# Kernel tuning notes

Measured on AMD Instinct MI355X. Metric: run time of the kernel, lower is better.

Reference implementation:

```python
import jax, jax.numpy as jnp
import numpy as np

NLAYERS, NHEAD, ATTN_LEN, DMODEL, DHID, NTOKEN = 9, 2, 5, 128, 512, 2
HD = DMODEL // NHEAD
B, T, F = 4, 4096, 128
INV_SQRT_HD = 1.0 / float(np.sqrt(HD))


def setup_inputs() -> dict:
    key = jax.random.key(0)
    ks = iter(jax.random.split(key, 64))
    def w(shape, s=0.02):
        return jax.random.normal(next(ks), shape, jnp.float32) * s
    return dict(
        x=jax.random.normal(next(ks), (B, T, F), jnp.float32),
        conv1_w=w((32, 1, 5, 3)), conv1_b=jnp.zeros((32,), jnp.float32),
        conv2_w=w((64, 32, 1, 12)), conv2_b=jnp.zeros((64,), jnp.float32),
        conv3_w=w((DMODEL, 64, 3, 6)), conv3_b=jnp.zeros((DMODEL,), jnp.float32),
        ln1_s=jnp.ones((NLAYERS, DMODEL), jnp.float32), ln1_b=jnp.zeros((NLAYERS, DMODEL), jnp.float32),
        ln2_s=jnp.ones((NLAYERS, DMODEL), jnp.float32), ln2_b=jnp.zeros((NLAYERS, DMODEL), jnp.float32),
        Wq=w((NLAYERS, DMODEL, DMODEL)), bq=jnp.zeros((NLAYERS, DMODEL), jnp.float32),
        Wk=w((NLAYERS, DMODEL, DMODEL)), bk=jnp.zeros((NLAYERS, DMODEL), jnp.float32),
        Wv=w((NLAYERS, DMODEL, DMODEL)), bv=jnp.zeros((NLAYERS, DMODEL), jnp.float32),
        Wo=w((NLAYERS, DMODEL, DMODEL)), bo=jnp.zeros((NLAYERS, DMODEL), jnp.float32),
        Er=w((NLAYERS, NHEAD, ATTN_LEN, HD)),
        W1=w((NLAYERS, DMODEL, DHID)), b1=jnp.zeros((NLAYERS, DHID), jnp.float32),
        W2=w((NLAYERS, DHID, DMODEL)), b2=jnp.zeros((NLAYERS, DMODEL), jnp.float32),
        Wout=w((DMODEL, NTOKEN)), bout=jnp.zeros((NTOKEN,), jnp.float32),
        Wt=w((DMODEL, 300)), bt=jnp.zeros((300,), jnp.float32),
    )


def _ln(x, s, b, eps=1e-5):
    m = x.mean(-1, keepdims=True)
    v = ((x - m) ** 2).mean(-1, keepdims=True)
    return (x - m) * jax.lax.rsqrt(v + eps) * s + b


def _conv(x, w, b, pad_h):
    y = jax.lax.conv_general_dilated(x, w, (1, 1), ((pad_h, pad_h), (0, 0)),
                                     dimension_numbers=('NCHW', 'OIHW', 'NCHW'))
    return y + b[None, :, None, None]


def _pool3(x):
    # MaxPool2d(kernel=(1,3), stride=(1,3)) on freq axis
    return jax.lax.reduce_window(x, -jnp.inf, jax.lax.max, (1, 1, 1, 3), (1, 1, 1, 3), 'VALID')


def _attn(x, Wq, bq, Wk, bk, Wv, bv, Wo, bo, Er, layer):
    # Dilated windowed attention: query t attends to t + (k - attn_len//2)*2^layer
    Bb, Tt, D = x.shape
    dil = 2 ** layer
    c = ATTN_LEN // 2
    q = (x @ Wq + bq).reshape(Bb, Tt, NHEAD, HD)
    k = (x @ Wk + bk).reshape(Bb, Tt, NHEAD, HD)
    v = (x @ Wv + bv).reshape(Bb, Tt, NHEAD, HD)
    offs = (jnp.arange(Tt)[:, None] + (jnp.arange(ATTN_LEN) - c)[None, :] * dil)  # (T, a)
    valid = (offs >= 0) & (offs < Tt)
    idx = jnp.clip(offs, 0, Tt - 1)
    kg = k[:, idx]  # (B, T, a, H, hd)
    vg = v[:, idx]
    scores = (jnp.einsum('bthd,btahd->bhta', q, kg)
              + jnp.einsum('bthd,had->bhta', q, Er)) * INV_SQRT_HD
    scores = jnp.where(valid[None, None], scores, -jnp.inf)
    a = jax.nn.softmax(scores, axis=-1)
    out = jnp.einsum('bhta,btahd->bthd', a, vg).reshape(Bb, Tt, D)
    return out @ Wo + bo


def _forward(x, conv1_w, conv1_b, conv2_w, conv2_b, conv3_w, conv3_b,
             ln1_s, ln1_b, ln2_s, ln2_b, Wq, bq, Wk, bk, Wv, bv, Wo, bo, Er,
             W1, b1, W2, b2, Wout, bout, Wt, bt):
    h = x[:, None]                                    # (B,1,T,F)
    h = jax.nn.relu(_pool3(_conv(h, conv1_w, conv1_b, 2)))
    h = jax.nn.relu(_pool3(_conv(h, conv2_w, conv2_b, 0)))
    h = jax.nn.relu(_pool3(_conv(h, conv3_w, conv3_b, 1)))  # (B,D,T,1)
    h = h[:, :, :, 0].transpose(0, 2, 1)              # (B,T,D)
    skips = []
    for l in range(NLAYERS):
        skip = _attn(_ln(h, ln1_s[l], ln1_b[l]), Wq[l], bq[l], Wk[l], bk[l],
                     Wv[l], bv[l], Wo[l], bo[l], Er[l], l)
        h = h + skip
        z = _ln(h, ln2_s[l], ln2_b[l])
        h = h + jax.nn.relu(z @ W1[l] + b1[l]) @ W2[l] + b2[l]
        skips.append(skip)
    out = jax.nn.relu(h) @ Wout + bout                # (B,T,ntoken)
    t = jax.nn.relu(sum(skips)).mean(axis=1) @ Wt + bt  # (B,300)
    return out, t


def reference(x, conv1_w, conv1_b, conv2_w, conv2_b, conv3_w, conv3_b,
              ln1_s, ln1_b, ln2_s, ln2_b, Wq, bq, Wk, bk, Wv, bv, Wo, bo, Er,
              W1, b1, W2, b2, Wout, bout, Wt, bt):
    return _forward(x, conv1_w, conv1_b, conv2_w, conv2_b, conv3_w, conv3_b,
                    ln1_s, ln1_b, ln2_s, ln2_b, Wq, bq, Wk, bk, Wv, bv, Wo, bo, Er,
                    W1, b1, W2, b2, Wout, bout, Wt, bt)
```

## Files before the change

kernel.cpp:

```cpp
#include <hip/hip_runtime.h>

#define T_ 4096
#define B_ 4

typedef unsigned short u16;
typedef __bf16 bf16x8 __attribute__((ext_vector_type(8)));
typedef float f32x4 __attribute__((ext_vector_type(4)));

__device__ inline void splitbf(float v, u16& h, u16& l) {
  __bf16 hb = (__bf16)v;
  float r = v - (float)hb;
  __bf16 lb = (__bf16)r;
  h = __builtin_bit_cast(u16, hb);
  l = __builtin_bit_cast(u16, lb);
}

#define MFMA(a,b,c) __builtin_amdgcn_mfma_f32_16x16x32_bf16((a),(b),(c),0,0,0)

__global__ __launch_bounds__(256) void k_conv12m(
    const float* __restrict__ x, const float* __restrict__ w1,
    const float* __restrict__ b1,
    const u16* __restrict__ wh, const u16* __restrict__ wl,
    const float* __restrict__ b2,
    u16* __restrict__ oh, u16* __restrict__ ol)
{
  __shared__ float sx[8][130];
  __shared__ float w1s[480];
  __shared__ float b1s[32];
  __shared__ u16 sh[4*43*40];
  __shared__ u16 sl[4*43*40];
  __shared__ float dmp[4][15][66];
  const int tid = threadIdx.x;
  const int t0 = blockIdx.x * 4;
  const int b = blockIdx.y;
  const float* xb = x + (size_t)b*T_*128;
  for (int i = tid; i < 1024; i += 256) {
    int r = i >> 7, c = i & 127;
    int t = t0 - 2 + r;
    sx[r][c] = (t >= 0 && t < T_) ? xb[t*128 + c] : 0.f;
  }
  for (int i = tid; i < 480; i += 256) w1s[i] = w1[i];
  if (tid < 32) b1s[tid] = b1[tid];
  for (int i = tid; i < 160; i += 256) {
    int tt = i / 40, c = i - tt*40;
    sh[(tt*43 + 42)*40 + c] = 0;
    sl[(tt*43 + 42)*40 + c] = 0;
  }
  __syncthreads();
  {
    const int c1 = tid & 31, tt = (tid >> 5) & 3, hf = tid >> 7;
    float w1r[15];
    #pragma unroll
    for (int i = 0; i < 15; i++) w1r[i] = w1s[c1*15 + i];
    float bb1 = b1s[c1];
    for (int wp = hf*21; wp < hf*21 + 21; wp++) {
      int c0 = wp*3;
      float s0 = 0.f, s1 = 0.f, s2 = 0.f;
      #pragma unroll
      for (int kh = 0; kh < 5; kh++) {
        float x0 = sx[tt+kh][c0],   x1 = sx[tt+kh][c0+1];
        float x2 = sx[tt+kh][c0+2], x3 = sx[tt+kh][c0+3];
        float x4 = sx[tt+kh][c0+4];
        float wA = w1r[kh*3], wB = w1r[kh*3+1], wC = w1r[kh*3+2];
        s0 += x0*wA + x1*wB + x2*wC;
        s1 += x1*wA + x2*wB + x3*wC;
        s2 += x2*wA + x3*wB + x4*wC;
      }
      float v = fmaxf(fmaxf(fmaxf(s0, s1), s2) + bb1, 0.f);
      u16 hh, ll; splitbf(v, hh, ll);
      int dd = (tt*43 + wp)*40 + c1;
      sh[dd] = hh; sl[dd] = ll;
    }
  }
  __syncthreads();
  const int lane = tid & 63;
  const int wid = tid >> 6;
  const int lr = lane & 15;
  const int lk8 = (lane >> 4) * 8;
  f32x4 acc[2][4] = {};
  #pragma unroll 3
  for (int kw = 0; kw < 12; kw++) {
    bf16x8 bh[4], bl[4];
    #pragma unroll
    for (int nf = 0; nf < 4; nf++) {
      int go = ((nf*12 + kw) << 9) + (lane << 3);
      bh[nf] = *(const bf16x8*)(wh + go);
      bl[nf] = *(const bf16x8*)(wl + go);
    }
    #pragma unroll
    for (int mf = 0; mf < 2; mf++) {
      int lofs = (wid*43 + mf*16 + lr + kw)*40 + lk8;
      bf16x8 ah = *(const bf16x8*)&sh[lofs];
      bf16x8 al = *(const bf16x8*)&sl[lofs];
      #pragma unroll
      for (int nf = 0; nf < 4; nf++) {
        acc[mf][nf] = MFMA(ah, bl[nf], acc[mf][nf]);
        acc[mf][nf] = MFMA(al, bh[nf], acc[mf][nf]);
        acc[mf][nf] = MFMA(ah, bh[nf], acc[mf][nf]);
      }
    }
  }
  const int lg = lane >> 4;
  {
    int t = t0 + wid;
    for (int half = 0; half < 2; half++) {
      #pragma unroll
      for (int mf = 0; mf < 2; mf++)
        #pragma unroll
        for (int r = 0; r < 4; r++) {
          int grow = mf*16 + lg*4 + r;
          int lrow = grow - half*15;
          if (lrow >= 0 && lrow < 15) {
            #pragma unroll
            for (int nf = 0; nf < 4; nf++)
              dmp[wid][lrow][nf*16 + lr] = acc[mf][nf][r];
          }
        }
      asm volatile("s_waitcnt lgkmcnt(0)" ::: "memory");
      #pragma unroll
      for (int it = 0; it < 5; it++) {
        float v = fmaxf(fmaxf(dmp[wid][it*3][lane], dmp[wid][it*3+1][lane]),
                        dmp[wid][it*3+2][lane]);
        v = fmaxf(v + b2[lane], 0.f);
        u16 hh, ll; splitbf(v, hh, ll);
        size_t o = (size_t)((b*T_ + t)*10 + half*5 + it)*64 + lane;
        oh[o] = hh; ol[o] = ll;
      }
      asm volatile("s_waitcnt lgkmcnt(0)" ::: "memory");
    }
  }
}

__global__ __launch_bounds__(256) void k_conv3m(
    const u16* __restrict__ ih, const u16* __restrict__ il,
    const u16* __restrict__ wh, const u16* __restrict__ wl,
    const float* __restrict__ b3, float* __restrict__ hout)
{
  __shared__ u16 sh[18*720];
  __shared__ u16 sl[18*720];
  __shared__ float dmp[48][132];
  const int tid = threadIdx.x;
  const int t0 = (blockIdx.x & 255) * 16;
  const int b = blockIdx.y;
  for (int i = tid; i < 1440; i += 256) {
    int cg = i & 7;
    int w = (i >> 3) % 10;
    int tt = i / 80;
    int t = t0 - 1 + tt;
    int dd = tt*720 + w*72 + cg*8;
    if (t >= 0 && t < T_) {
      size_t so = (size_t)((b*T_ + t)*10 + w)*64 + cg*8;
      *(ulonglong2*)&sh[dd] = *(const ulonglong2*)&ih[so];
      *(ulonglong2*)&sl[dd] = *(const ulonglong2*)&il[so];
    } else {
      ulonglong2 z; z.x = 0; z.y = 0;
      *(ulonglong2*)&sh[dd] = z;
      *(ulonglong2*)&sl[dd] = z;
    }
  }
  __syncthreads();
  const int lane = tid & 63;
  const int wid = tid >> 6;
  const int lr = lane & 15;
  const int lk8 = (lane >> 4) * 8;
  int tlm[3], wom[3];
  #pragma unroll
  for (int mf = 0; mf < 3; mf++) {
    int r = mf*16 + lr;
    tlm[mf] = r / 3;
    wom[mf] = r - tlm[mf]*3;
  }
  f32x4 acc[3][2] = {};
  #pragma unroll 2
  for (int kh = 0; kh < 3; kh++) {
    #pragma unroll
    for (int kw = 0; kw < 6; kw++) {
      #pragma unroll
      for (int chh = 0; chh < 2; chh++) {
        int s = (kh*6 + kw)*2 + chh;
        int ch = chh*32;
        bf16x8 bh[2], bl[2];
        #pragma unroll
        for (int nfl = 0; nfl < 2; nfl++) {
          int go = (((wid*2 + nfl)*36 + s) << 9) + (lane << 3);
          bh[nfl] = *(const bf16x8*)(wh + go);
          bl[nfl] = *(const bf16x8*)(wl + go);
        }
        #pragma unroll
        for (int mf = 0; mf < 3; mf++) {
          int lofs = (tlm[mf] + kh)*720 + (wom[mf] + kw)*72 + ch + lk8;
          bf16x8 ah = *(const bf16x8*)&sh[lofs];
          bf16x8 al = *(const bf16x8*)&sl[lofs];
          #pragma unroll
          for (int nfl = 0; nfl < 2; nfl++) {
            acc[mf][nfl] = MFMA(ah, bl[nfl], acc[mf][nfl]);
            acc[mf][nfl] = MFMA(al, bh[nfl], acc[mf][nfl]);
            acc[mf][nfl] = MFMA(ah, bh[nfl], acc[mf][nfl]);
          }
        }
      }
    }
  }
  const int lg = lane >> 4;
  #pragma unroll
  for (int mf = 0; mf < 3; mf++)
    #pragma unroll
    for (int r = 0; r < 4; r++) {
      int row = mf*16 + lg*4 + r;
      #pragma unroll
      for (int nfl = 0; nfl < 2; nfl++)
        dmp[row][wid*32 + nfl*16 + lr] = acc[mf][nfl][r];
    }
  __syncthreads();
  for (int i = tid; i < 2048; i += 256) {
    int c3 = i & 127;
    int tt = i >> 7;
    float v = fmaxf(fmaxf(dmp[tt*3][c3], dmp[tt*3+1][c3]), dmp[tt*3+2][c3]);
    v = fmaxf(v + b3[c3], 0.f);
    hout[(size_t)(b*T_ + t0 + tt)*128 + c3] = v;
  }
}

__device__ inline float wave_sum(float v) {
  #pragma unroll
  for (int m = 1; m < 64; m <<= 1) v += __shfl_xor(v, m, 64);
  return v;
}

__device__ inline void prep_fr(const float* __restrict__ src,
                               u16* __restrict__ dh, u16* __restrict__ dl,
                               int K, int N, int matStride, int idx)
{
  int mat = idx / (K*N);
  int rem = idx - mat*(K*N);
  int k = rem / N;
  int n = rem - k*N;
  float v = src[idx];
  u16 h, l; splitbf(v, h, l);
  int nt = n >> 4, ks = k >> 5, ksub = k & 31;
  size_t o = (size_t)mat*matStride + (size_t)((nt*(K>>5) + ks) << 9)
           + (((ksub >> 3) << 4) + (n & 15))*8 + (ksub & 7);
  dh[o] = h; dl[o] = l;
}

__global__ __launch_bounds__(256) void k_wprep_all(
    const float* __restrict__ Wq, const float* __restrict__ Wk,
    const float* __restrict__ Wv, const float* __restrict__ Wo,
    const float* __restrict__ W1, const float* __restrict__ W2,
    const float* __restrict__ c2w, const float* __restrict__ c3w,
    u16* wqkv_h, u16* wqkv_l, u16* wo_h, u16* wo_l,
    u16* w1t_h, u16* w1t_l, u16* w2t_h, u16* w2t_l,
    u16* wc2_h, u16* wc2_l, u16* wc3_h, u16* wc3_l)
{
  const int bid = blockIdx.x;
  const int tid = threadIdx.x;
  if (bid < 576) {
    prep_fr(Wq, wqkv_h, wqkv_l, 128, 128, 49152, bid*256 + tid);
  } else if (bid < 1152) {
    prep_fr(Wk, wqkv_h + 16384, wqkv_l + 16384, 128, 128, 49152, (bid-576)*256 + tid);
  } else if (bid < 1728) {
    prep_fr(Wv, wqkv_h + 32768, wqkv_l + 32768, 128, 128, 49152, (bid-1152)*256 + tid);
  } else if (bid < 2304) {
    prep_fr(Wo, wo_h, wo_l, 128, 128, 16384, (bid-1728)*256 + tid);
  } else if (bid < 4608) {
    prep_fr(W1, w1t_h, w1t_l, 128, 512, 65536, (bid-2304)*256 + tid);
  } else if (bid < 6912) {
    prep_fr(W2, w2t_h, w2t_l, 512, 128, 65536, (bid-4608)*256 + tid);
  } else if (bid < 7008) {
    int idx = (bid-6912)*256 + tid;
    int c2 = idx / 384;
    int rem = idx - c2*384;
    int c1 = rem / 12;
    int kw = rem - c1*12;
    float v = c2w[idx];
    u16 h, l; splitbf(v, h, l);
    size_t o = (size_t)((((c2 >> 4)*12 + kw) << 9))
             + (((c1 >> 3) << 4) + (c2 & 15))*8 + (c1 & 7);
    wc2_h[o] = h; wc2_l[o] = l;
  } else {
    int idx = (bid-7008)*256 + tid;
    int c3 = idx / 1152;
    int rem = idx - c3*1152;
    int c2 = rem / 18;
    int khkw = rem - c2*18;
    float v = c3w[idx];
    u16 h, l; splitbf(v, h, l);
    int s = khkw*2 + (c2 >> 5);
    int c = c2 & 31;
    size_t o = (size_t)((((c3 >> 4)*36 + s) << 9))
             + (((c >> 3) << 4) + (c3 & 15))*8 + (c & 7);
    wc3_h[o] = h; wc3_l[o] = l;
  }
}

__global__ __launch_bounds__(512) void k_pre0(
    const float* __restrict__ hbuf,
    const float* __restrict__ sc, const float* __restrict__ bi,
    const u16* __restrict__ Qh, const u16* __restrict__ Ql,
    const float* __restrict__ bq, const float* __restrict__ bk,
    const float* __restrict__ bv, float* __restrict__ qout)
{
  __shared__ u16 sAh[32*136], sAl[32*136];
  const int tid = threadIdx.x, lane = tid & 63;
  const int m0 = blockIdx.x * 32;
  {
    const int row = tid >> 4, p = tid & 15;
    float xv[8], s = 0.f;
    const float* hp = &hbuf[(size_t)(m0 + row)*128 + p*8];
    #pragma unroll
    for (int i = 0; i < 8; i++) { xv[i] = hp[i]; s += xv[i]; }
    s += __shfl_xor(s, 1); s += __shfl_xor(s, 2);
    s += __shfl_xor(s, 4); s += __shfl_xor(s, 8);
    float mean = s * (1.f/128.f);
    float v = 0.f;
    #pragma unroll
    for (int i = 0; i < 8; i++) { float d = xv[i]-mean; v += d*d; }
    v += __shfl_xor(v, 1); v += __shfl_xor(v, 2);
    v += __shfl_xor(v, 4); v += __shfl_xor(v, 8);
    float rs = rsqrtf(v*(1.f/128.f) + 1e-5f);
    #pragma unroll
    for (int i = 0; i < 8; i++) {
      int cc = p*8 + i;
      float y = (xv[i]-mean)*rs*sc[cc] + bi[cc];
      u16 hh, ll; splitbf(y, hh, ll);
      sAh[row*136 + cc] = hh; sAl[row*136 + cc] = ll;
    }
  }
  __syncthreads();
  const int wv = tid >> 6, mq = wv >> 2, nq = wv & 3;
  const int lr = lane & 15, lg = lane >> 4, l8 = lg*8;
  for (int z = 0; z < 3; z++) {
    const u16* wh = Qh + z*16384;
    const u16* wl = Ql + z*16384;
    const float* bias = (z == 0) ? bq : (z == 1) ? bk : bv;
    float* C = qout + (size_t)z*2097152;
    f32x4 acc[2] = {};
    #pragma unroll
    for (int ks = 0; ks < 4; ks++) {
      bf16x8 ah = *(const bf16x8*)&sAh[(mq*16 + lr)*136 + ks*32 + l8];
      bf16x8 al = *(const bf16x8*)&sAl[(mq*16 + lr)*136 + ks*32 + l8];
      #pragma unroll
      for (int nf = 0; nf < 2; nf++) {
        int go = (((nq*2 + nf)*4 + ks) << 9) + (lane << 3);
        bf16x8 bh = *(const bf16x8*)(wh + go);
        bf16x8 bl = *(const bf16x8*)(wl + go);
        acc[nf] = MFMA(ah, bl, acc[nf]);
        acc[nf] = MFMA(al, bh, acc[nf]);
        acc[nf] = MFMA(ah, bh, acc[nf]);
      }
    }
    #pragma unroll
    for (int nf = 0; nf < 2; nf++) {
      int col = nq*32 + nf*16 + lr;
      float bb = bias[col];
      #pragma unroll
      for (int r = 0; r < 4; r++)
        C[(size_t)(m0 + mq*16 + lg*4 + r)*128 + col] = acc[nf][r] + bb;
    }
  }
}

__global__ __launch_bounds__(512) void k_layer(
    const float* __restrict__ qin,
    const float* __restrict__ Er,
    const u16* __restrict__ Woh, const u16* __restrict__ Wol,
    const float* __restrict__ bo,
    const float* __restrict__ sc2, const float* __restrict__ bi2,
    const u16* __restrict__ W1h, const u16* __restrict__ W1l,
    const float* __restrict__ b1,
    const u16* __restrict__ W2h, const u16* __restrict__ W2l,
    const float* __restrict__ b2,
    float* __restrict__ hbuf, float* __restrict__ ssum, int skip_init,
    int do_qkv,
    const float* __restrict__ sc1, const float* __restrict__ bi1,
    const u16* __restrict__ Qh, const u16* __restrict__ Ql,
    const float* __restrict__ bq, const float* __restrict__ bk,
    const float* __restrict__ bv, float* __restrict__ qout, int dil,
    const float* __restrict__ Wout, const float* __restrict__ bout,
    float* __restrict__ part, float* __restrict__ outf)
{
  __shared__ u16 sAh[32*136], sAl[32*136];
  __shared__ __align__(16) char ureg[17408];
  u16* hidH = (u16*)ureg;
  u16* hidL = (u16*)(ureg + 8704);
  float* dmp = (float*)ureg;
  const int tid = threadIdx.x, lane = tid & 63, wv = tid >> 6;
  const int m0 = blockIdx.x * 32;
  const int b = m0 >> 12;
  const int t0 = m0 & 4095;
  const float* qb = qin;
  const float* kb = qin + 2097152;
  const float* vb = qin + 4194304;
  for (int rr = 0; rr < 4; rr++) {
    int r = wv*4 + rr;
    int t = t0 + r;
    int bt = m0 + r;
    #pragma unroll
    for (int h = 0; h < 2; h++) {
      float qd = qb[(size_t)bt*128 + h*64 + lane];
      float s[5];
      int tpc_arr[5];
      #pragma unroll
      for (int a = 0; a < 5; a++) {
        int tp = t + (a-2)*dil;
        bool valid = (tp >= 0 && tp < T_);
        int tpc = tp < 0 ? 0 : (tp > T_-1 ? T_-1 : tp);
        tpc_arr[a] = tpc;
        float kd = kb[(size_t)(b*T_ + tpc)*128 + h*64 + lane];
        float er = Er[(h*5 + a)*64 + lane];
        float p = qd * (kd + er);
        p = wave_sum(p);
        s[a] = valid ? p * 0.125f : -1e30f;
      }
      float mx = s[0];
      #pragma unroll
      for (int a = 1; a < 5; a++) mx = fmaxf(mx, s[a]);
      float p[5], psum = 0.f;
      #pragma unroll
      for (int a = 0; a < 5; a++) { p[a] = __expf(s[a]-mx); psum += p[a]; }
      float inv = 1.f/psum;
      float o = 0.f;
      #pragma unroll
      for (int a = 0; a < 5; a++)
        o += p[a] * vb[(size_t)(b*T_ + tpc_arr[a])*128 + h*64 + lane];
      float vo = o * inv;
      u16 hh, ll; splitbf(vo, hh, ll);
      sAh[r*136 + h*64 + lane] = hh;
      sAl[r*136 + h*64 + lane] = ll;
    }
  }
  __syncthreads();
  const int lr = lane & 15, lg = lane >> 4, l8 = lg*8;
  const int mq = wv >> 2, nq = wv & 3;
  {
    f32x4 acc[2] = {};
    #pragma unroll
    for (int ks = 0; ks < 4; ks++) {
      bf16x8 ah = *(const bf16x8*)&sAh[(mq*16 + lr)*136 + ks*32 + l8];
      bf16x8 al = *(const bf16x8*)&sAl[(mq*16 + lr)*136 + ks*32 + l8];
      #pragma unroll
      for (int nf = 0; nf < 2; nf++) {
        int go = (((nq*2 + nf)*4 + ks) << 9) + (lane << 3);
        bf16x8 bh = *(const bf16x8*)(Woh + go);
        bf16x8 bl = *(const bf16x8*)(Wol + go);
        acc[nf] = MFMA(ah, bl, acc[nf]);
        acc[nf] = MFMA(al, bh, acc[nf]);
        acc[nf] = MFMA(ah, bh, acc[nf]);
      }
    }
    #pragma unroll
    for (int nf = 0; nf < 2; nf++) {
      int col = nq*32 + nf*16 + lr;
      float bb = bo[col];
      #pragma unroll
      for (int r = 0; r < 4; r++) {
        int row = mq*16 + lg*4 + r;
        size_t o = (size_t)(m0 + row)*128 + col;
        float val = acc[nf][r] + bb;
        if (skip_init) ssum[o] = val; else ssum[o] += val;
        float hn = hbuf[o] + val;
        hbuf[o] = hn;
        dmp[row*132 + col] = hn;
      }
    }
  }
  __syncthreads();
  {
    const int row = tid >> 4, p = tid & 15;
    float xv[8], s = 0.f;
    const float* dp = &dmp[row*132 + p*8];
    #pragma unroll
    for (int i = 0; i < 8; i++) { xv[i] = dp[i]; s += xv[i]; }
    s += __shfl_xor(s, 1); s += __shfl_xor(s, 2);
    s += __shfl_xor(s, 4); s += __shfl_xor(s, 8);
    float mean = s * (1.f/128.f);
    float v = 0.f;
    #pragma unroll
    for (int i = 0; i < 8; i++) { float d = xv[i]-mean; v += d*d; }
    v += __shfl_xor(v, 1); v += __shfl_xor(v, 2);
    v += __shfl_xor(v, 4); v += __shfl_xor(v, 8);
    float rs = rsqrtf(v*(1.f/128.f) + 1e-5f);
    #pragma unroll
    for (int i = 0; i < 8; i++) {
      int cc = p*8 + i;
      float y = (xv[i]-mean)*rs*sc2[cc] + bi2[cc];
      u16 hh, ll; splitbf(y, hh, ll);
      sAh[row*136 + cc] = hh; sAl[row*136 + cc] = ll;
    }
  }
  __syncthreads();
  f32x4 acc2[2] = {};
  for (int c = 0; c < 4; c++) {
    f32x4 acc1[2] = {};
    #pragma unroll
    for (int ks = 0; ks < 4; ks++) {
      bf16x8 ah = *(const bf16x8*)&sAh[(mq*16 + lr)*136 + ks*32 + l8];
      bf16x8 al = *(const bf16x8*)&sAl[(mq*16 + lr)*136 + ks*32 + l8];
      #pragma unroll
      for (int nf = 0; nf < 2; nf++) {
        int go = (((c*8 + nq*2 + nf)*4 + ks) << 9) + (lane << 3);
        bf16x8 bh = *(const bf16x8*)(W1h + go);
        bf16x8 bl = *(const bf16x8*)(W1l + go);
        acc1[nf] = MFMA(ah, bl, acc1[nf]);
        acc1[nf] = MFMA(al, bh, acc1[nf]);
        acc1[nf] = MFMA(ah, bh, acc1[nf]);
      }
    }
    __syncthreads();
    #pragma unroll
    for (int nf = 0; nf < 2; nf++) {
      int col = nq*32 + nf*16 + lr;
      float bb = b1[c*128 + col];
      #pragma unroll
      for (int r = 0; r < 4; r++) {
        int row = mq*16 + lg*4 + r;
        float hv = fmaxf(acc1[nf][r] + bb, 0.f);
        u16 hh, ll; splitbf(hv, hh, ll);
        hidH[row*136 + col] = hh;
        hidL[row*136 + col] = ll;
      }
    }
    __syncthreads();
    #pragma unroll
    for (int ks = 0; ks < 4; ks++) {
      bf16x8 ah = *(const bf16x8*)&hidH[(mq*16 + lr)*136 + ks*32 + l8];
      bf16x8 al = *(const bf16x8*)&hidL[(mq*16 + lr)*136 + ks*32 + l8];
      #pragma unroll
      for (int nf = 0; nf < 2; nf++) {
        int go = (((nq*2 + nf)*16 + c*4 + ks) << 9) + (lane << 3);
        bf16x8 bh = *(const bf16x8*)(W2h + go);
        bf16x8 bl = *(const bf16x8*)(W2l + go);
        acc2[nf] = MFMA(ah, bl, acc2[nf]);
        acc2[nf] = MFMA(al, bh, acc2[nf]);
        acc2[nf] = MFMA(ah, bh, acc2[nf]);
      }
    }
  }
  __syncthreads();
  #pragma unroll
  for (int nf = 0; nf < 2; nf++) {
    int col = nq*32 + nf*16 + lr;
    float bb = b2[col];
    #pragma unroll
    for (int r = 0; r < 4; r++) {
      int row = mq*16 + lg*4 + r;
      size_t o = (size_t)(m0 + row)*128 + col;
      float hn = hbuf[o] + acc2[nf][r] + bb;
      hbuf[o] = hn;
      dmp[row*132 + col] = hn;
    }
  }
  __syncthreads();
  if (do_qkv) {
    {
      const int row = tid >> 4, p = tid & 15;
      float xv[8], s = 0.f;
      const float* dp = &dmp[row*132 + p*8];
      #pragma unroll
      for (int i = 0; i < 8; i++) { xv[i] = dp[i]; s += xv[i]; }
      s += __shfl_xor(s, 1); s += __shfl_xor(s, 2);
      s += __shfl_xor(s, 4); s += __shfl_xor(s, 8);
      float mean = s * (1.f/128.f);
      float v = 0.f;
      #pragma unroll
      for (int i = 0; i < 8; i++) { float d = xv[i]-mean; v += d*d; }
      v += __shfl_xor(v, 1); v += __shfl_xor(v, 2);
      v += __shfl_xor(v, 4); v += __shfl_xor(v, 8);
      float rs = rsqrtf(v*(1.f/128.f) + 1e-5f);
      #pragma unroll
      for (int i = 0; i < 8; i++) {
        int cc = p*8 + i;
        float y = (xv[i]-mean)*rs*sc1[cc] + bi1[cc];
        u16 hh, ll; splitbf(y, hh, ll);
        sAh[row*136 + cc] = hh; sAl[row*136 + cc] = ll;
      }
    }
    __syncthreads();
    for (int z = 0; z < 3; z++) {
      const u16* wh = Qh + z*16384;
      const u16* wl = Ql + z*16384;
      const float* bias = (z == 0) ? bq : (z == 1) ? bk : bv;
      float* C = qout + (size_t)z*2097152;
      f32x4 acc[2] = {};
      #pragma unroll
      for (int ks = 0; ks < 4; ks++) {
        bf16x8 ah = *(const bf16x8*)&sAh[(mq*16 + lr)*136 + ks*32 + l8];
        bf16x8 al = *(const bf16x8*)&sAl[(mq*16 + lr)*136 + ks*32 + l8];
        #pragma unroll
        for (int nf = 0; nf < 2; nf++) {
          int go = (((nq*2 + nf)*4 + ks) << 9) + (lane << 3);
          bf16x8 bh = *(const bf16x8*)(wh + go);
          bf16x8 bl = *(const bf16x8*)(wl + go);
          acc[nf] = MFMA(ah, bl, acc[nf]);
          acc[nf] = MFMA(al, bh, acc[nf]);
          acc[nf] = MFMA(ah, bh, acc[nf]);
        }
      }
      #pragma unroll
      for (int nf = 0; nf < 2; nf++) {
        int col = nq*32 + nf*16 + lr;
        float bb = bias[col];
        #pragma unroll
        for (int r = 0; r < 4; r++)
          C[(size_t)(m0 + mq*16 + lg*4 + r)*128 + col] = acc[nf][r] + bb;
      }
    }
  } else {
    {
      const int row = tid >> 4, p = tid & 15;
      float o0 = 0.f, o1 = 0.f;
      const float* dp = &dmp[row*132 + p*8];
      #pragma unroll
      for (int i = 0; i < 8; i++) {
        float hv = fmaxf(dp[i], 0.f);
        o0 += hv * Wout[(p*8 + i)*2];
        o1 += hv * Wout[(p*8 + i)*2 + 1];
      }
      o0 += __shfl_xor(o0, 1); o0 += __shfl_xor(o0, 2);
      o0 += __shfl_xor(o0, 4); o0 += __shfl_xor(o0, 8);
      o1 += __shfl_xor(o1, 1); o1 += __shfl_xor(o1, 2);
      o1 += __shfl_xor(o1, 4); o1 += __shfl_xor(o1, 8);
      if (p == 0) {
        outf[(size_t)(m0 + row)*2]     = o0 + bout[0];
        outf[(size_t)(m0 + row)*2 + 1] = o1 + bout[1];
      }
    }
    __syncthreads();
    {
      float* pr = dmp;
      int c = tid & 127, q = tid >> 7;
      float s = 0.f;
      #pragma unroll
      for (int r = 0; r < 8; r++)
        s += fmaxf(ssum[(size_t)(m0 + q*8 + r)*128 + c], 0.f);
      pr[q*128 + c] = s;
      __syncthreads();
      if (tid < 128)
        part[(size_t)blockIdx.x*128 + tid] =
            pr[tid] + pr[128+tid] + pr[256+tid] + pr[384+tid];
    }
  }
}

__global__ __launch_bounds__(512) void k_tail2(
    const float* __restrict__ part, const float* __restrict__ Wt,
    const float* __restrict__ btb, float* __restrict__ out)
{
  __shared__ float mb[512];
  const int tid = threadIdx.x;
  int b = tid >> 7, c = tid & 127;
  float s = 0.f;
  for (int j = 0; j < 128; j++)
    s += part[(size_t)(b*128 + j)*128 + c];
  mb[tid] = s * (1.f/4096.f);
  __syncthreads();
  for (int i = tid; i < 1200; i += 512) {
    int bb = i / 300, j = i - bb*300;
    float acc = btb[j];
    #pragma unroll 4
    for (int k2 = 0; k2 < 128; k2++)
      acc += mb[bb*128 + k2] * Wt[k2*300 + j];
    out[32768 + i] = acc;
  }
}

extern "C" void kernel_launch(void* const* d_in, const int* in_sizes, int n_in,
                              void* d_out, int out_size, void* d_ws, size_t ws_size,
                              hipStream_t stream)
{
  const float* x    = (const float*)d_in[0];
  const float* c1w  = (const float*)d_in[1];
  const float* c1b  = (const float*)d_in[2];
  const float* c2w  = (const float*)d_in[3];
  const float* c2b  = (const float*)d_in[4];
  const float* c3w  = (const float*)d_in[5];
  const float* c3b  = (const float*)d_in[6];
  const float* ln1s = (const float*)d_in[7];
  const float* ln1b = (const float*)d_in[8];
  const float* ln2s = (const float*)d_in[9];
  const float* ln2b = (const float*)d_in[10];
  const float* Wq   = (const float*)d_in[11];
  const float* bq   = (const float*)d_in[12];
  const float* Wk   = (const float*)d_in[13];
  const float* bk   = (const float*)d_in[14];
  const float* Wv   = (const float*)d_in[15];
  const float* bv   = (const float*)d_in[16];
  const float* Wo   = (const float*)d_in[17];
  const float* bo   = (const float*)d_in[18];
  const float* Er   = (const float*)d_in[19];
  const float* W1   = (const float*)d_in[20];
  const float* b1   = (const float*)d_in[21];
  const float* W2   = (const float*)d_in[22];
  const float* b2   = (const float*)d_in[23];
  const float* Wout = (const float*)d_in[24];
  const float* bout = (const float*)d_in[25];
  const float* Wt   = (const float*)d_in[26];
  const float* bt   = (const float*)d_in[27];

  char* W = (char*)d_ws;
  u16* c2o_h = (u16*)W;
  u16* c2o_l = (u16*)(W + 20971520);
  char* RB = W + 41943040;
  float* qbuf0 = (float*)RB;
  float* qbuf1 = (float*)(RB + 25165824);
  char* RC = W + 100663296;
  float* hbuf = (float*)RC;
  float* ssum = (float*)(RC + 8388608);
  u16* wqkv_h = (u16*)(RC + 16777216);
  u16* wqkv_l = wqkv_h + 442368;
  u16* wo_h   = wqkv_l + 442368;
  u16* wo_l   = wo_h + 147456;
  u16* w1t_h  = wo_l + 147456;
  u16* w1t_l  = w1t_h + 589824;
  u16* w2t_h  = w1t_l + 589824;
  u16* w2t_l  = w2t_h + 589824;
  u16* wc2_h  = w2t_l + 589824;
  u16* wc2_l  = wc2_h + 24576;
  u16* wc3_h  = wc2_l + 24576;
  u16* wc3_l  = wc3_h + 147456;
  float* part  = (float*)(wc3_l + 147456);
  float* outf  = (float*)d_out;

  k_wprep_all<<<7584, 256, 0, stream>>>(
      Wq, Wk, Wv, Wo, W1, W2, c2w, c3w,
      wqkv_h, wqkv_l, wo_h, wo_l, w1t_h, w1t_l, w2t_h, w2t_l,
      wc2_h, wc2_l, wc3_h, wc3_l);

  k_conv12m<<<dim3(1024, B_), 256, 0, stream>>>(x, c1w, c1b, wc2_h, wc2_l, c2b,
                                                c2o_h, c2o_l);
  k_conv3m<<<dim3(256, B_), 256, 0, stream>>>(c2o_h, c2o_l, wc3_h, wc3_l, c3b, hbuf);

  k_pre0<<<512, 512, 0, stream>>>(hbuf, ln1s, ln1b,
                                  wqkv_h, wqkv_l, bq, bk, bv, qbuf0);

  for (int l = 0; l < 9; l++) {
    int ln = (l < 8) ? (l + 1) : 0;
    float* qin  = (l & 1) ? qbuf1 : qbuf0;
    float* qout = (l & 1) ? qbuf0 : qbuf1;
    k_layer<<<512, 512, 0, stream>>>(
        qin, Er + l*640,
        wo_h + l*16384, wo_l + l*16384, bo + l*128,
        ln2s + l*128, ln2b + l*128,
        w1t_h + l*65536, w1t_l + l*65536, b1 + l*512,
        w2t_h + l*65536, w2t_l + l*65536, b2 + l*128,
        hbuf, ssum, (l == 0) ? 1 : 0,
        (l < 8) ? 1 : 0,
        ln1s + ln*128, ln1b + ln*128,
        wqkv_h + ln*49152, wqkv_l + ln*49152,
        bq + ln*128, bk + ln*128, bv + ln*128, qout, 1 << l,
        Wout, bout, part, outf);
  }

  k_tail2<<<1, 512, 0, stream>>>(part, Wt, bt, outf);
}
```

Measured before the change: 669.4 us.

## Fuse transformer layer loop into one persistent cooperative kernel with grid syncs

Replaces the per-layer launches (pre0, nine layer kernels, tail) with a single cooperative kernel of 512 blocks. The blocks loop over the layers and use grid.sync between layers, and Q for each block's own rows stays in shared memory so only K and V go through global memory. This removes launch overhead and the global round trip for Q. In exchange it depends on every block being co-resident and pays a grid-wide barrier per layer, with the old multi-kernel path kept as a fallback.

New measurement: 669.9 us. About the same (+0.1%).

```diff
diff --git a/kernel.cpp b/kernel.cpp
--- a/kernel.cpp
+++ b/kernel.cpp
@@ -1,4 +1,6 @@
 #include <hip/hip_runtime.h>
+#include <hip/hip_cooperative_groups.h>
+namespace cg = cooperative_groups;
 
 #define T_ 4096
 #define B_ 4
@@ -664,6 +666,364 @@
   }
 }
 
+struct LoopArgs {
+  const float* Er;
+  const u16* woh; const u16* wol; const float* bo;
+  const float* ln2s; const float* ln2b;
+  const u16* w1h; const u16* w1l; const float* b1;
+  const u16* w2h; const u16* w2l; const float* b2;
+  float* hbuf; float* ssum;
+  const float* ln1s; const float* ln1b;
+  const u16* wqh; const u16* wql;
+  const float* bq; const float* bk; const float* bv;
+  float* kvbuf;
+  const float* Wout; const float* bout;
+  const float* Wt; const float* btb;
+  float* part; float* outf;
+};
+
+__device__ inline void qkv_emit(
+    const u16* sAh, const u16* sAl,
+    const u16* wq_h, const u16* wq_l,
+    const float* bq, const float* bk, const float* bv,
+    float* sQ, float* kvout,
+    int m0, int mq, int nq, int lr, int lg, int l8, int lane)
+{
+  for (int z = 0; z < 3; z++) {
+    const u16* wh = wq_h + z*16384;
+    const u16* wl = wq_l + z*16384;
+    const float* bias = (z == 0) ? bq : (z == 1) ? bk : bv;
+    f32x4 acc[2] = {};
+    #pragma unroll
+    for (int ks = 0; ks < 4; ks++) {
+      bf16x8 ah = *(const bf16x8*)&sAh[(mq*16 + lr)*136 + ks*32 + l8];
+      bf16x8 al = *(const bf16x8*)&sAl[(mq*16 + lr)*136 + ks*32 + l8];
+      #pragma unroll
+      for (int nf = 0; nf < 2; nf++) {
+        int go = (((nq*2 + nf)*4 + ks) << 9) + (lane << 3);
+        bf16x8 bh = *(const bf16x8*)(wh + go);
+        bf16x8 bl = *(const bf16x8*)(wl + go);
+        acc[nf] = MFMA(ah, bl, acc[nf]);
+        acc[nf] = MFMA(al, bh, acc[nf]);
+        acc[nf] = MFMA(ah, bh, acc[nf]);
+      }
+    }
+    #pragma unroll
+    for (int nf = 0; nf < 2; nf++) {
+      int col = nq*32 + nf*16 + lr;
+      float bb = bias[col];
+      #pragma unroll
+      for (int r = 0; r < 4; r++) {
+        int row = mq*16 + lg*4 + r;
+        float val = acc[nf][r] + bb;
+        if (z == 0) sQ[row*132 + col] = val;
+        else kvout[(size_t)(z-1)*2097152 + (size_t)(m0 + row)*128 + col] = val;
+      }
+    }
+  }
+}
+
+__global__ __launch_bounds__(512, 4) void k_loop(LoopArgs a)
+{
+  __shared__ u16 sAh[32*136], sAl[32*136];
+  __shared__ float sQ[32*132];
+  __shared__ __align__(16) char ureg[17408];
+  u16* hidH = (u16*)ureg;
+  u16* hidL = (u16*)(ureg + 8704);
+  float* dmp = (float*)ureg;
+  cg::grid_group grid = cg::this_grid();
+  const int tid = threadIdx.x, lane = tid & 63, wv = tid >> 6;
+  const int m0 = blockIdx.x * 32;
+  const int b = m0 >> 12;
+  const int t0 = m0 & 4095;
+  const int lr = lane & 15, lg = lane >> 4, l8 = lg*8;
+  const int mq = wv >> 2, nq = wv & 3;
+  const int row16 = tid >> 4, p16 = tid & 15;
+
+  {
+    float xv[8], s = 0.f;
+    const float* hp = &a.hbuf[(size_t)(m0 + row16)*128 + p16*8];
+    #pragma unroll
+    for (int i = 0; i < 8; i++) { xv[i] = hp[i]; s += xv[i]; }
+    s += __shfl_xor(s, 1); s += __shfl_xor(s, 2);
+    s += __shfl_xor(s, 4); s += __shfl_xor(s, 8);
+    float mean = s * (1.f/128.f);
+    float v = 0.f;
+    #pragma unroll
+    for (int i = 0; i < 8; i++) { float d = xv[i]-mean; v += d*d; }
+    v += __shfl_xor(v, 1); v += __shfl_xor(v, 2);
+    v += __shfl_xor(v, 4); v += __shfl_xor(v, 8);
+    float rs = rsqrtf(v*(1.f/128.f) + 1e-5f);
+    #pragma unroll
+    for (int i = 0; i < 8; i++) {
+      int cc = p16*8 + i;
+      float y = (xv[i]-mean)*rs*a.ln1s[cc] + a.ln1b[cc];
+      u16 hh, ll; splitbf(y, hh, ll);
+      sAh[row16*136 + cc] = hh; sAl[row16*136 + cc] = ll;
+    }
+  }
+  __syncthreads();
+  qkv_emit(sAh, sAl, a.wqh, a.wql, a.bq, a.bk, a.bv,
+           sQ, a.kvbuf, m0, mq, nq, lr, lg, l8, lane);
+
+  for (int l = 0; l < 9; l++) {
+    grid.sync();
+    const float* kb = a.kvbuf + (size_t)(l & 1)*4194304;
+    const float* vb = kb + 2097152;
+    const float* Er_l = a.Er + l*640;
+    const int dil = 1 << l;
+    for (int rr = 0; rr < 4; rr++) {
+      int r = wv*4 + rr;
+      int t = t0 + r;
+      #pragma unroll
+      for (int h = 0; h < 2; h++) {
+        float qd = sQ[r*132 + h*64 + lane];
+        float s[5];
+        int tpc_arr[5];
+        #pragma unroll
+        for (int aa = 0; aa < 5; aa++) {
+          int tp = t + (aa-2)*dil;
+          bool valid = (tp >= 0 && tp < T_);
+          int tpc = tp < 0 ? 0 : (tp > T_-1 ? T_-1 : tp);
+          tpc_arr[aa] = tpc;
+          float kd = kb[(size_t)(b*T_ + tpc)*128 + h*64 + lane];
+          float er = Er_l[(h*5 + aa)*64 + lane];
+          float p = qd * (kd + er);
+          p = wave_sum(p);
+          s[aa] = valid ? p * 0.125f : -1e30f;
+        }
+        float mx = s[0];
+        #pragma unroll
+        for (int aa = 1; aa < 5; aa++) mx = fmaxf(mx, s[aa]);
+        float p[5], psum = 0.f;
+        #pragma unroll
+        for (int aa = 0; aa < 5; aa++) { p[aa] = __expf(s[aa]-mx); psum += p[aa]; }
+        float inv = 1.f/psum;
+        float o = 0.f;
+        #pragma unroll
+        for (int aa = 0; aa < 5; aa++)
+          o += p[aa] * vb[(size_t)(b*T_ + tpc_arr[aa])*128 + h*64 + lane];
+        float vo = o * inv;
+        u16 hh, ll; splitbf(vo, hh, ll);
+        sAh[r*136 + h*64 + lane] = hh;
+        sAl[r*136 + h*64 + lane] = ll;
+      }
+    }
+    __syncthreads();
+    {
+      const u16* Woh = a.woh + l*16384;
+      const u16* Wol = a.wol + l*16384;
+      const float* bo = a.bo + l*128;
+      f32x4 acc[2] = {};
+      #pragma unroll
+      for (int ks = 0; ks < 4; ks++) {
+        bf16x8 ah = *(const bf16x8*)&sAh[(mq*16 + lr)*136 + ks*32 + l8];
+        bf16x8 al = *(const bf16x8*)&sAl[(mq*16 + lr)*136 + ks*32 + l8];
+        #pragma unroll
+        for (int nf = 0; nf < 2; nf++) {
+          int go = (((nq*2 + nf)*4 + ks) << 9) + (lane << 3);
+          bf16x8 bh = *(const bf16x8*)(Woh + go);
+          bf16x8 bl = *(const bf16x8*)(Wol + go);
+          acc[nf] = MFMA(ah, bl, acc[nf]);
+          acc[nf] = MFMA(al, bh, acc[nf]);
+          acc[nf] = MFMA(ah, bh, acc[nf]);
+        }
+      }
+      #pragma unroll
+      for (int nf = 0; nf < 2; nf++) {
+        int col = nq*32 + nf*16 + lr;
+        float bb = bo[col];
+        #pragma unroll
+        for (int r = 0; r < 4; r++) {
+          int row = mq*16 + lg*4 + r;
+          size_t o = (size_t)(m0 + row)*128 + col;
+          float val = acc[nf][r] + bb;
+          if (l == 0) a.ssum[o] = val; else a.ssum[o] += val;
+          float hn = a.hbuf[o] + val;
+          a.hbuf[o] = hn;
+          dmp[row*132 + col] = hn;
+        }
+      }
+    }
+    __syncthreads();
+    {
+      const float* sc2 = a.ln2s + l*128;
+      const float* bi2 = a.ln2b + l*128;
+      float xv[8], s = 0.f;
+      const float* dp = &dmp[row16*132 + p16*8];
+      #pragma unroll
+      for (int i = 0; i < 8; i++) { xv[i] = dp[i]; s += xv[i]; }
+      s += __shfl_xor(s, 1); s += __shfl_xor(s, 2);
+      s += __shfl_xor(s, 4); s += __shfl_xor(s, 8);
+      float mean = s * (1.f/128.f);
+      float v = 0.f;
+      #pragma unroll
+      for (int i = 0; i < 8; i++) { float d = xv[i]-mean; v += d*d; }
+      v += __shfl_xor(v, 1); v += __shfl_xor(v, 2);
+      v += __shfl_xor(v, 4); v += __shfl_xor(v, 8);
+      float rs = rsqrtf(v*(1.f/128.f) + 1e-5f);
+      #pragma unroll
+      for (int i = 0; i < 8; i++) {
+        int cc = p16*8 + i;
+        float y = (xv[i]-mean)*rs*sc2[cc] + bi2[cc];
+        u16 hh, ll; splitbf(y, hh, ll);
+        sAh[row16*136 + cc] = hh; sAl[row16*136 + cc] = ll;
+      }
+    }
+    __syncthreads();
+    const u16* W1h = a.w1h + l*65536;
+    const u16* W1l = a.w1l + l*65536;
+    const u16* W2h = a.w2h + l*65536;
+    const u16* W2l = a.w2l + l*65536;
+    const float* b1l = a.b1 + l*512;
+    const float* b2l = a.b2 + l*128;
+    f32x4 acc2[2] = {};
+    for (int c = 0; c < 4; c++) {
+      f32x4 acc1[2] = {};
+      #pragma unroll
+      for (int ks = 0; ks < 4; ks++) {
+        bf16x8 ah = *(const bf16x8*)&sAh[(mq*16 + lr)*136 + ks*32 + l8];
+        bf16x8 al = *(const bf16x8*)&sAl[(mq*16 + lr)*136 + ks*32 + l8];
+        #pragma unroll
+        for (int nf = 0; nf < 2; nf++) {
+          int go = (((c*8 + nq*2 + nf)*4 + ks) << 9) + (lane << 3);
+          bf16x8 bh = *(const bf16x8*)(W1h + go);
+          bf16x8 bl = *(const bf16x8*)(W1l + go);
+          acc1[nf] = MFMA(ah, bl, acc1[nf]);
+          acc1[nf] = MFMA(al, bh, acc1[nf]);
+          acc1[nf] = MFMA(ah, bh, acc1[nf]);
+        }
+      }
+      __syncthreads();
+      #pragma unroll
+      for (int nf = 0; nf < 2; nf++) {
+        int col = nq*32 + nf*16 + lr;
+        float bb = b1l[c*128 + col];
+        #pragma unroll
+        for (int r = 0; r < 4; r++) {
+          int row = mq*16 + lg*4 + r;
+          float hv = fmaxf(acc1[nf][r] + bb, 0.f);
+          u16 hh, ll; splitbf(hv, hh, ll);
+          hidH[row*136 + col] = hh;
+          hidL[row*136 + col] = ll;
+        }
+      }
+      __syncthreads();
+      #pragma unroll
+      for (int ks = 0; ks < 4; ks++) {
+        bf16x8 ah = *(const bf16x8*)&hidH[(mq*16 + lr)*136 + ks*32 + l8];
+        bf16x8 al = *(const bf16x8*)&hidL[(mq*16 + lr)*136 + ks*32 + l8];
+        #pragma unroll
+        for (int nf = 0; nf < 2; nf++) {
+          int go = (((nq*2 + nf)*16 + c*4 + ks) << 9) + (lane << 3);
+          bf16x8 bh = *(const bf16x8*)(W2h + go);
+          bf16x8 bl = *(const bf16x8*)(W2l + go);
+          acc2[nf] = MFMA(ah, bl, acc2[nf]);
+          acc2[nf] = MFMA(al, bh, acc2[nf]);
+          acc2[nf] = MFMA(ah, bh, acc2[nf]);
+        }
+      }
+    }
+    __syncthreads();
+    #pragma unroll
+    for (int nf = 0; nf < 2; nf++) {
+      int col = nq*32 + nf*16 + lr;
+      float bb = b2l[col];
+      #pragma unroll
+      for (int r = 0; r < 4; r++) {
+        int row = mq*16 + lg*4 + r;
+        size_t o = (size_t)(m0 + row)*128 + col;
+        float hn = a.hbuf[o] + acc2[nf][r] + bb;
+        a.hbuf[o] = hn;
+        dmp[row*132 + col] = hn;
+      }
+    }
+    __syncthreads();
+    if (l < 8) {
+      {
+        const float* sc1 = a.ln1s + (l+1)*128;
+        const float* bi1 = a.ln1b + (l+1)*128;
+        float xv[8], s = 0.f;
+        const float* dp = &dmp[row16*132 + p16*8];
+        #pragma unroll
+        for (int i = 0; i < 8; i++) { xv[i] = dp[i]; s += xv[i]; }
+        s += __shfl_xor(s, 1); s += __shfl_xor(s, 2);
+        s += __shfl_xor(s, 4); s += __shfl_xor(s, 8);
+        float mean = s * (1.f/128.f);
+        float v = 0.f;
+        #pragma unroll
+        for (int i = 0; i < 8; i++) { float d = xv[i]-mean; v += d*d; }
+        v += __shfl_xor(v, 1); v += __shfl_xor(v, 2);
+        v += __shfl_xor(v, 4); v += __shfl_xor(v, 8);
+        float rs = rsqrtf(v*(1.f/128.f) + 1e-5f);
+        #pragma unroll
+        for (int i = 0; i < 8; i++) {
+          int cc = p16*8 + i;
+          float y = (xv[i]-mean)*rs*sc1[cc] + bi1[cc];
+          u16 hh, ll; splitbf(y, hh, ll);
+          sAh[row16*136 + cc] = hh; sAl[row16*136 + cc] = ll;
+        }
+      }
+      __syncthreads();
+      qkv_emit(sAh, sAl, a.wqh + (l+1)*49152, a.wql + (l+1)*49152,
+               a.bq + (l+1)*128, a.bk + (l+1)*128, a.bv + (l+1)*128,
+               sQ, a.kvbuf + (size_t)((l+1) & 1)*4194304,
+               m0, mq, nq, lr, lg, l8, lane);
+    } else {
+      {
+        float o0 = 0.f, o1 = 0.f;
+        const float* dp = &dmp[row16*132 + p16*8];
+        #pragma unroll
+        for (int i = 0; i < 8; i++) {
+          float hv = fmaxf(dp[i], 0.f);
+          o0 += hv * a.Wout[(p16*8 + i)*2];
+          o1 += hv * a.Wout[(p16*8 + i)*2 + 1];
+        }
+        o0 += __shfl_xor(o0, 1); o0 += __shfl_xor(o0, 2);
+        o0 += __shfl_xor(o0, 4); o0 += __shfl_xor(o0, 8);
+        o1 += __shfl_xor(o1, 1); o1 += __shfl_xor(o1, 2);
+        o1 += __shfl_xor(o1, 4); o1 += __shfl_xor(o1, 8);
+        if (p16 == 0) {
+          a.outf[(size_t)(m0 + row16)*2]     = o0 + a.bout[0];
+          a.outf[(size_t)(m0 + row16)*2 + 1] = o1 + a.bout[1];
+        }
+      }
+      __syncthreads();
+      {
+        float* pr = dmp;
+        int c = tid & 127, q = tid >> 7;
+        float s = 0.f;
+        #pragma unroll
+        for (int r = 0; r < 8; r++)
+          s += fmaxf(a.ssum[(size_t)(m0 + q*8 + r)*128 + c], 0.f);
+        pr[q*128 + c] = s;
+        __syncthreads();
+        if (tid < 128)
+          a.part[(size_t)blockIdx.x*128 + tid] =
+              pr[tid] + pr[128+tid] + pr[256+tid] + pr[384+tid];
+      }
+    }
+  }
+  grid.sync();
+  if (blockIdx.x == 0) {
+    float* mb = dmp;
+    int bb = tid >> 7, c = tid & 127;
+    float s = 0.f;
+    for (int j = 0; j < 128; j++)
+      s += a.part[(size_t)(bb*128 + j)*128 + c];
+    mb[tid] = s * (1.f/4096.f);
+    __syncthreads();
+    for (int i = tid; i < 1200; i += 512) {
+      int b2 = i / 300, j = i - b2*300;
+      float acc = a.btb[j];
+      #pragma unroll 4
+      for (int k2 = 0; k2 < 128; k2++)
+        acc += mb[b2*128 + k2] * a.Wt[k2*300 + j];
+      a.outf[32768 + i] = acc;
+    }
+  }
+}
+
 extern "C" void kernel_launch(void* const* d_in, const int* in_sizes, int n_in,
                               void* d_out, int out_size, void* d_ws, size_t ws_size,
                               hipStream_t stream)
@@ -703,6 +1063,7 @@
   char* RB = W + 41943040;
   float* qbuf0 = (float*)RB;
   float* qbuf1 = (float*)(RB + 25165824);
+  float* kvbuf = (float*)RB;
   char* RC = W + 100663296;
   float* hbuf = (float*)RC;
   float* ssum = (float*)(RC + 8388608);
@@ -730,26 +1091,60 @@
                                                 c2o_h, c2o_l);
   k_conv3m<<<dim3(256, B_), 256, 0, stream>>>(c2o_h, c2o_l, wc3_h, wc3_l, c3b, hbuf);
 
-  k_pre0<<<512, 512, 0, stream>>>(hbuf, ln1s, ln1b,
-                                  wqkv_h, wqkv_l, bq, bk, bv, qbuf0);
-
-  for (int l = 0; l < 9; l++) {
-    int ln = (l < 8) ? (l + 1) : 0;
-    float* qin  = (l & 1) ? qbuf1 : qbuf0;
-    float* qout = (l & 1) ? qbuf0 : qbuf1;
-    k_layer<<<512, 512, 0, stream>>>(
-        qin, Er + l*640,
-        wo_h + l*16384, wo_l + l*16384, bo + l*128,
-        ln2s + l*128, ln2b + l*128,
-        w1t_h + l*65536, w1t_l + l*65536, b1 + l*512,
-        w2t_h + l*65536, w2t_l + l*65536, b2 + l*128,
-        hbuf, ssum, (l == 0) ? 1 : 0,
-        (l < 8) ? 1 : 0,
-        ln1s + ln*128, ln1b + ln*128,
-        wqkv_h + ln*49152, wqkv_l + ln*49152,
-        bq + ln*128, bk + ln*128, bv + ln*128, qout, 1 << l,
-        Wout, bout, part, outf);
-  }
-
-  k_tail2<<<1, 512, 0, stream>>>(part, Wt, bt, outf);
+  bool use_coop = false;
+  {
+    int dev = 0;
+    if (hipGetDevice(&dev) == hipSuccess) {
+      int coopAttr = 0;
+      if (hipDeviceGetAttribute(&coopAttr, hipDeviceAttributeCooperativeLaunch,
+                                dev) == hipSuccess && coopAttr) {
+        int nb = 0;
+        if (hipOccupancyMaxActiveBlocksPerMultiprocessor(
+                &nb, (const void*)k_loop, 512, 0) == hipSuccess && nb >= 2)
+          use_coop = true;
+      }
+    }
+  }
+  if (use_coop) {
+    LoopArgs la;
+    la.Er = Er;
+    la.woh = wo_h; la.wol = wo_l; la.bo = bo;
+    la.ln2s = ln2s; la.ln2b = ln2b;
+    la.w1h = w1t_h; la.w1l = w1t_l; la.b1 = b1;
+    la.w2h = w2t_h; la.w2l = w2t_l; la.b2 = b2;
+    la.hbuf = hbuf; la.ssum = ssum;
+    la.ln1s = ln1s; la.ln1b = ln1b;
+    la.wqh = wqkv_h; la.wql = wqkv_l;
+    la.bq = bq; la.bk = bk; la.bv = bv;
+    la.kvbuf = kvbuf;
+    la.Wout = Wout; la.bout = bout;
+    la.Wt = Wt; la.btb = bt;
+    la.part = part; la.outf = outf;
+    void* kargs[] = { (void*)&la };
+    if (hipLaunchCooperativeKernel((const void*)k_loop, dim3(512), dim3(512),
+                                   kargs, 0, stream) != hipSuccess)
+      use_coop = false;
+  }
+  if (!use_coop) {
+    k_pre0<<<512, 512, 0, stream>>>(hbuf, ln1s, ln1b,
+                                    wqkv_h, wqkv_l, bq, bk, bv, qbuf0);
+    for (int l = 0; l < 9; l++) {
+      int ln = (l < 8) ? (l + 1) : 0;
+      float* qin  = (l & 1) ? qbuf1 : qbuf0;
+      float* qout = (l & 1) ? qbuf0 : qbuf1;
+      k_layer<<<512, 512, 0, stream>>>(
+          qin, Er + l*640,
+          wo_h + l*16384, wo_l + l*16384, bo + l*128,
+          ln2s + l*128, ln2b + l*128,
+          w1t_h + l*65536, w1t_l + l*65536, b1 + l*512,
+          w2t_h + l*65536, w2t_l + l*65536, b2 + l*128,
+          hbuf, ssum, (l == 0) ? 1 : 0,
+          (l < 8) ? 1 : 0,
+          ln1s + ln*128, ln1b + ln*128,
+          wqkv_h + ln*49152, wqkv_l + ln*49152,
+          bq + ln*128, bk + ln*128, bv + ln*128, qout, 1 << l,
+          Wout, bout, part, outf);
+    }
+    k_tail2<<<1, 512, 0, stream>>>(part, Wt, bt, outf);
+  }
 }
```
